# Performance work log

Measured on AMD Instinct MI355X. Metric: run time of the kernel, lower is better.

Reference implementation:

```python
import jax, jax.numpy as jnp
import numpy as np

G, N, F, H, L, B = 8, 1024, 128, 256, 4, 64


def setup_inputs() -> dict:
    key = jax.random.key(0)
    ks = jax.random.split(key, 8)
    graph = jax.random.randint(ks[0], (B,), 0, G)
    # boolean coverpoint mask; force column 0 True so no row is empty
    mask = jax.random.uniform(ks[1], (B, N)) < 0.2
    mask = mask.at[:, 0].set(True)
    cdfg_xs = jax.random.normal(ks[2], (G, N, F), dtype=jnp.float32)
    cdfg_as = (jax.random.uniform(ks[3], (G, N, N)) < 0.02).astype(jnp.float32) / 20.0
    W_in = jax.random.normal(ks[4], (F, H), dtype=jnp.float32) * (1.0 / np.sqrt(F))
    b_in = jnp.zeros((H,), dtype=jnp.float32)
    Ws = jax.random.normal(ks[5], (L, H, H), dtype=jnp.float32) * (1.0 / np.sqrt(H))
    bs = jnp.zeros((L, H), dtype=jnp.float32)
    return {"graph": graph, "coverpoint_mask": mask, "cdfg_xs": cdfg_xs,
            "cdfg_as": cdfg_as, "W_in": W_in, "b_in": b_in, "Ws": Ws, "bs": bs}


def reference(graph, coverpoint_mask, cdfg_xs, cdfg_as, W_in, b_in, Ws, bs):
    # gather per-sample graphs (tf.gather_nd equivalent)
    xs = cdfg_xs[graph]          # [B, N, F]
    As = cdfg_as[graph]          # [B, N, N]
    # input Dense with relu
    x = jax.nn.relu(jnp.einsum('bnf,fh->bnh', xs, W_in) + b_in)  # [B, N, H]
    to_add = x
    n_layers = Ws.shape[0]
    for i in range(n_layers):
        h = jnp.einsum('bnm,bmh->bnh', As, jnp.einsum('bnh,hk->bnk', x, Ws[i])) + bs[i]
        if i == n_layers - 1:
            x = jax.nn.softmax(h, axis=-1)   # final_activation='softmax'
        else:
            x = jax.nn.relu(h)
    x = x + to_add
    # ragged boolean_mask + reduce_mean over nodes == masked mean
    m = coverpoint_mask[..., None].astype(x.dtype)   # [B, N, 1]
    s = jnp.sum(x * m, axis=1)                       # [B, H]
    cnt = jnp.maximum(jnp.sum(m, axis=1), 1.0)
    return s / cnt
```

## Files before the change

### kernel.cpp

```cpp
#include <hip/hip_runtime.h>
#include <hip/hip_bf16.h>

#define GG 8
#define NN 1024
#define FF 128
#define HH 256
#define LL 4
#define BB 64
#define MM (GG * NN)

typedef __attribute__((ext_vector_type(8))) short bf16x8_t;
typedef __attribute__((ext_vector_type(4))) float f32x4_t;

__device__ inline unsigned short f2bf(float f) {
  union { float f; unsigned u; } c;
  c.f = f;
  unsigned r = (c.u + 0x7fffu + ((c.u >> 16) & 1u)) >> 16;
  return (unsigned short)r;
}

__global__ void detect_mask_kernel(const uint4* __restrict__ mb,
                                   int* __restrict__ flags) {
  const int i = blockIdx.x * blockDim.x + threadIdx.x;
  const uint4 v = mb[i];
  const unsigned all = v.x | v.y | v.z | v.w;
  const int nonz = (all & 0xFFFFFF00u) != 0;
  const int isf32 = ((v.x >> 24) == 0x3fu) || ((v.y >> 24) == 0x3fu) ||
                    ((v.z >> 24) == 0x3fu) || ((v.w >> 24) == 0x3fu);
  const unsigned long long bn = __ballot(nonz);
  const unsigned long long bf = __ballot(isf32);
  if ((threadIdx.x & 63) == 0) {
    if (bn) atomicOr(&flags[0], 1);
    if (bf) atomicOr(&flags[1], 1);
  }
}

__global__ __launch_bounds__(256) void convert_xs_kernel(
    const float4* __restrict__ in, ushort4* __restrict__ out) {
  const int i = blockIdx.x * 256 + threadIdx.x;
  const float4 v = in[i];
  ushort4 o;
  o.x = f2bf(v.x); o.y = f2bf(v.y); o.z = f2bf(v.z); o.w = f2bf(v.w);
  out[i] = o;
}

__global__ __launch_bounds__(256) void convert_w_kernel(
    const float* __restrict__ W_in, const float* __restrict__ Ws,
    unsigned short* __restrict__ WinT, unsigned short* __restrict__ WsT) {
  const int idx = blockIdx.x * 256 + threadIdx.x;
  if (idx < FF * HH) {
    const int n = idx >> 7, k = idx & (FF - 1);
    WinT[idx] = f2bf(W_in[k * HH + n]);
  } else {
    const int j = idx - FF * HH;
    const int l = j >> 16, n = (j >> 8) & 255, k = j & 255;
    WsT[j] = f2bf(Ws[((size_t)l * HH + k) * HH + n]);
  }
}

template <int K, bool FUSED>
__global__ __launch_bounds__(256) void mfma_gemm_kernel(
    const unsigned short* __restrict__ A, const unsigned short* __restrict__ BT,
    const float* __restrict__ bias, unsigned short* __restrict__ Cb,
    float* __restrict__ Cf) {
  __shared__ uint4 As4[4 * 64];
  __shared__ uint4 Bs4[4 * 64];
  const int t = threadIdx.x;
  const int lane = t & 63;
  const int w = t >> 6;
  const int wm = (w >> 1) * 32;
  const int wn = (w & 1) * 32;
  const int m0 = blockIdx.x * 64;
  const int n0 = blockIdx.y * 64;
  const int srow = t >> 2;
  const int skseg = t & 3;
  const int lk = lane >> 4;
  const int lr = lane & 15;
  f32x4_t acc[2][2] = {};
  for (int k0 = 0; k0 < K; k0 += 32) {
    As4[skseg * 64 + srow] =
        *(const uint4*)(A + (size_t)(m0 + srow) * K + k0 + skseg * 8);
    Bs4[skseg * 64 + srow] =
        *(const uint4*)(BT + (size_t)(n0 + srow) * K + k0 + skseg * 8);
    __syncthreads();
    const bf16x8_t a0 = *(const bf16x8_t*)(&As4[lk * 64 + wm + lr]);
    const bf16x8_t a1 = *(const bf16x8_t*)(&As4[lk * 64 + wm + 16 + lr]);
    const bf16x8_t b0 = *(const bf16x8_t*)(&Bs4[lk * 64 + wn + lr]);
    const bf16x8_t b1 = *(const bf16x8_t*)(&Bs4[lk * 64 + wn + 16 + lr]);
    acc[0][0] = __builtin_amdgcn_mfma_f32_16x16x32_bf16(a0, b0, acc[0][0], 0, 0, 0);
    acc[0][1] = __builtin_amdgcn_mfma_f32_16x16x32_bf16(a0, b1, acc[0][1], 0, 0, 0);
    acc[1][0] = __builtin_amdgcn_mfma_f32_16x16x32_bf16(a1, b0, acc[1][0], 0, 0, 0);
    acc[1][1] = __builtin_amdgcn_mfma_f32_16x16x32_bf16(a1, b1, acc[1][1], 0, 0, 0);
    __syncthreads();
  }
#pragma unroll
  for (int rg = 0; rg < 2; ++rg)
#pragma unroll
    for (int cg = 0; cg < 2; ++cg)
#pragma unroll
      for (int j = 0; j < 4; ++j) {
        const int row = m0 + wm + rg * 16 + (lane >> 4) * 4 + j;
        const int col = n0 + wn + cg * 16 + lr;
        float v = acc[rg][cg][j];
        if (FUSED) {
          v += bias[col];
          v = fmaxf(v, 0.0f);
          Cb[(size_t)row * HH + col] = f2bf(v);
          Cf[(size_t)row * HH + col] = v;
        } else {
          Cf[(size_t)row * HH + col] = v;
        }
      }
}

__global__ __launch_bounds__(256) void spmm_kernel(
    const float* __restrict__ Adj, const float* __restrict__ Y,
    const float* __restrict__ bias, const float* __restrict__ X0,
    unsigned short* __restrict__ Xb, float* __restrict__ Xf, int final_layer) {
  const int lane = threadIdx.x & 63;
  const int wid = threadIdx.x >> 6;
  const int r = blockIdx.x * 4 + wid;
  const int g = r >> 10;
  const int n = r & (NN - 1);
  const float* __restrict__ Arow = Adj + ((size_t)g * NN + n) * NN;
  const float* __restrict__ Yg = Y + (size_t)g * NN * HH;
  float acc0 = 0.f, acc1 = 0.f, acc2 = 0.f, acc3 = 0.f;
  for (int mc = 0; mc < NN; mc += 64) {
    const float a = Arow[mc + lane];
    unsigned long long bal = __ballot(a != 0.0f);
    while (bal) {
      const int j = __builtin_ctzll(bal);
      bal &= bal - 1;
      const float v = __shfl(a, j);
      const float* __restrict__ Yrow = Yg + (size_t)(mc + j) * HH;
      acc0 += v * Yrow[lane];
      acc1 += v * Yrow[lane + 64];
      acc2 += v * Yrow[lane + 128];
      acc3 += v * Yrow[lane + 192];
    }
  }
  const float h0 = acc0 + bias[lane];
  const float h1 = acc1 + bias[lane + 64];
  const float h2 = acc2 + bias[lane + 128];
  const float h3 = acc3 + bias[lane + 192];
  const size_t rowoff = ((size_t)g * NN + n) * HH;
  if (!final_layer) {
    unsigned short* __restrict__ Xrow = Xb + rowoff;
    Xrow[lane] = f2bf(fmaxf(h0, 0.f));
    Xrow[lane + 64] = f2bf(fmaxf(h1, 0.f));
    Xrow[lane + 128] = f2bf(fmaxf(h2, 0.f));
    Xrow[lane + 192] = f2bf(fmaxf(h3, 0.f));
  } else {
    float mx = fmaxf(fmaxf(h0, h1), fmaxf(h2, h3));
#pragma unroll
    for (int off = 32; off >= 1; off >>= 1) mx = fmaxf(mx, __shfl_xor(mx, off));
    const float e0 = __expf(h0 - mx), e1 = __expf(h1 - mx);
    const float e2 = __expf(h2 - mx), e3 = __expf(h3 - mx);
    float s = e0 + e1 + e2 + e3;
#pragma unroll
    for (int off = 32; off >= 1; off >>= 1) s += __shfl_xor(s, off);
    const float inv = 1.0f / s;
    float* __restrict__ Xrow = Xf + rowoff;
    const float* __restrict__ X0row = X0 + rowoff;
    Xrow[lane] = e0 * inv + X0row[lane];
    Xrow[lane + 64] = e1 * inv + X0row[lane + 64];
    Xrow[lane + 128] = e2 * inv + X0row[lane + 128];
    Xrow[lane + 192] = e3 * inv + X0row[lane + 192];
  }
}

__global__ __launch_bounds__(256) void mm_partial_kernel(
    const float* __restrict__ X, const int* __restrict__ graph,
    const void* __restrict__ mask, const int* __restrict__ flags,
    float* __restrict__ partial, float* __restrict__ cntbuf) {
  __shared__ unsigned char m[64];
  const int c = blockIdx.x;
  const int b = blockIdx.y;
  const int h = threadIdx.x;
  const int n0 = c * 64;
  const int mode = flags[1] ? 2 : (flags[0] ? 0 : 1);
  if (h < 64) {
    const int n = n0 + h;
    bool on;
    if (mode == 1) on = ((const int*)mask)[(size_t)b * NN + n] != 0;
    else if (mode == 2) on = ((const float*)mask)[(size_t)b * NN + n] != 0.0f;
    else on = ((const unsigned char*)mask)[(size_t)b * NN + n] != 0;
    m[h] = on ? 1 : 0;
  }
  __syncthreads();
  const int g = graph[b];
  const float* __restrict__ Xg = X + ((size_t)g * NN + n0) * HH;
  float a0 = 0.f, a1 = 0.f, a2 = 0.f, a3 = 0.f;
  int c0 = 0, c1 = 0, c2 = 0, c3 = 0;
#pragma unroll 4
  for (int n = 0; n < 16; ++n) {
    if (m[n])      { a0 += Xg[(size_t)n * HH + h]; c0++; }
    if (m[n + 16]) { a1 += Xg[(size_t)(n + 16) * HH + h]; c1++; }
    if (m[n + 32]) { a2 += Xg[(size_t)(n + 32) * HH + h]; c2++; }
    if (m[n + 48]) { a3 += Xg[(size_t)(n + 48) * HH + h]; c3++; }
  }
  partial[((size_t)b * 16 + c) * HH + h] = (a0 + a1) + (a2 + a3);
  if (h == 0) cntbuf[b * 16 + c] = (float)((c0 + c1) + (c2 + c3));
}

__global__ __launch_bounds__(256) void mm_reduce_kernel(
    const float* __restrict__ partial, const float* __restrict__ cntbuf,
    float* __restrict__ out) {
  const int b = blockIdx.x, h = threadIdx.x;
  float s = 0.f;
#pragma unroll
  for (int c = 0; c < 16; ++c) s += partial[((size_t)b * 16 + c) * HH + h];
  float cnt = 0.f;
#pragma unroll
  for (int c = 0; c < 16; ++c) cnt += cntbuf[b * 16 + c];
  out[(size_t)b * HH + h] = s / fmaxf(cnt, 1.0f);
}

extern "C" void kernel_launch(void* const* d_in, const int* in_sizes, int n_in,
                              void* d_out, int out_size, void* d_ws,
                              size_t ws_size, hipStream_t stream) {
  const int* graph = (const int*)d_in[0];
  const void* mask = d_in[1];
  const float* xs = (const float*)d_in[2];
  const float* As = (const float*)d_in[3];
  const float* W_in = (const float*)d_in[4];
  const float* b_in = (const float*)d_in[5];
  const float* Ws = (const float*)d_in[6];
  const float* bs = (const float*)d_in[7];
  float* out = (float*)d_out;

  float* X = (float*)d_ws;
  float* X0 = X + (size_t)MM * HH;
  float* Y = X0 + (size_t)MM * HH;
  unsigned short* Xb = (unsigned short*)(Y + (size_t)MM * HH);
  unsigned short* xsb = Xb + (size_t)MM * HH;
  unsigned short* WinT = xsb + (size_t)MM * FF;
  unsigned short* WsT = WinT + (size_t)HH * FF;
  int* flags = (int*)(WsT + (size_t)LL * HH * HH);
  float* partial = Y;
  float* cntbuf = Y + BB * 16 * HH;

  hipMemsetAsync(flags, 0, 2 * sizeof(int), stream);
  detect_mask_kernel<<<16, 256, 0, stream>>>((const uint4*)mask, flags);
  convert_xs_kernel<<<MM * FF / 4 / 256, 256, 0, stream>>>((const float4*)xs,
                                                           (ushort4*)xsb);
  convert_w_kernel<<<(FF * HH + LL * HH * HH) / 256, 256, 0, stream>>>(
      W_in, Ws, WinT, WsT);

  const dim3 grd(MM / 64, HH / 64);
  mfma_gemm_kernel<FF, true><<<grd, 256, 0, stream>>>(xsb, WinT, b_in, Xb, X0);
  for (int i = 0; i < LL; ++i) {
    mfma_gemm_kernel<HH, false><<<grd, 256, 0, stream>>>(
        Xb, WsT + (size_t)i * HH * HH, nullptr, nullptr, Y);
    spmm_kernel<<<MM / 4, 256, 0, stream>>>(As, Y, bs + (size_t)i * HH, X0, Xb,
                                            X, (i == LL - 1) ? 1 : 0);
  }
  mm_partial_kernel<<<dim3(16, BB), 256, 0, stream>>>(X, graph, mask, flags,
                                                      partial, cntbuf);
  mm_reduce_kernel<<<BB, 256, 0, stream>>>(partial, cntbuf, out);
}
```

Measured before the change: 223.4 us.

## Build ELL adjacency once and gather bf16 intermediates in SpMM

Adds a kernel that scans the dense adjacency once per call and compacts each row's nonzeros into a fixed-capacity ELL list of value/column pairs plus a count. Each of the four layer SpMMs then walks this list instead of rescanning the full dense matrix. The per-layer GEMM output is now stored as bf16, and the SpMM gathers it with vectorized ushort4 loads and writes with float4/ushort4 stores, which halves gather traffic. The cost is an extra build pass, more workspace, and lower precision in the intermediate. Rows with more than 96 nonzeros would be silently truncated, which is safe only at this input density.

```diff
diff --git a/kernel.cpp b/kernel.cpp
--- a/kernel.cpp
+++ b/kernel.cpp
@@ -8,6 +8,7 @@
 #define LL 4
 #define BB 64
 #define MM (GG * NN)
+#define ELLCAP 96
 
 typedef __attribute__((ext_vector_type(8))) short bf16x8_t;
 typedef __attribute__((ext_vector_type(4))) float f32x4_t;
@@ -17,6 +18,11 @@
   c.f = f;
   unsigned r = (c.u + 0x7fffu + ((c.u >> 16) & 1u)) >> 16;
   return (unsigned short)r;
+}
+__device__ inline float bf2f(unsigned short u) {
+  union { unsigned u; float f; } c;
+  c.u = (unsigned)u << 16;
+  return c.f;
 }
 
 __global__ void detect_mask_kernel(const uint4* __restrict__ mb,
@@ -56,6 +62,31 @@
     const int l = j >> 16, n = (j >> 8) & 255, k = j & 255;
     WsT[j] = f2bf(Ws[((size_t)l * HH + k) * HH + n]);
   }
+}
+
+__global__ __launch_bounds__(256) void ell_build_kernel(
+    const float* __restrict__ Adj, uint2* __restrict__ ell,
+    int* __restrict__ cntArr) {
+  const int lane = threadIdx.x & 63;
+  const int wid = threadIdx.x >> 6;
+  const int r = blockIdx.x * 4 + wid;
+  const float* __restrict__ Arow = Adj + (size_t)r * NN;
+  int cnt = 0;
+  for (int mc = 0; mc < NN; mc += 64) {
+    const float a = Arow[mc + lane];
+    const unsigned long long bal = __ballot(a != 0.0f);
+    if (a != 0.0f) {
+      const int pos = cnt + __popcll(bal & ((1ULL << lane) - 1ULL));
+      if (pos < ELLCAP) {
+        uint2 e;
+        e.x = __float_as_uint(a);
+        e.y = (unsigned)(mc + lane);
+        ell[(size_t)r * ELLCAP + pos] = e;
+      }
+    }
+    cnt += __popcll(bal);
+  }
+  if (lane == 0) cntArr[r] = min(cnt, ELLCAP);
 }
 
 template <int K, bool FUSED>
@@ -108,48 +139,48 @@
           Cb[(size_t)row * HH + col] = f2bf(v);
           Cf[(size_t)row * HH + col] = v;
         } else {
-          Cf[(size_t)row * HH + col] = v;
+          Cb[(size_t)row * HH + col] = f2bf(v);
         }
       }
 }
 
-__global__ __launch_bounds__(256) void spmm_kernel(
-    const float* __restrict__ Adj, const float* __restrict__ Y,
-    const float* __restrict__ bias, const float* __restrict__ X0,
-    unsigned short* __restrict__ Xb, float* __restrict__ Xf, int final_layer) {
+__global__ __launch_bounds__(256) void spmm_ell_kernel(
+    const uint2* __restrict__ ell, const int* __restrict__ cntArr,
+    const unsigned short* __restrict__ Yb, const float* __restrict__ bias,
+    const float* __restrict__ X0, unsigned short* __restrict__ Xb,
+    float* __restrict__ Xf, int final_layer) {
   const int lane = threadIdx.x & 63;
   const int wid = threadIdx.x >> 6;
   const int r = blockIdx.x * 4 + wid;
   const int g = r >> 10;
-  const int n = r & (NN - 1);
-  const float* __restrict__ Arow = Adj + ((size_t)g * NN + n) * NN;
-  const float* __restrict__ Yg = Y + (size_t)g * NN * HH;
+  const unsigned short* __restrict__ Yg = Yb + (size_t)g * NN * HH;
+  const int cnt = cntArr[r];
+  const uint2* __restrict__ erow = ell + (size_t)r * ELLCAP;
   float acc0 = 0.f, acc1 = 0.f, acc2 = 0.f, acc3 = 0.f;
-  for (int mc = 0; mc < NN; mc += 64) {
-    const float a = Arow[mc + lane];
-    unsigned long long bal = __ballot(a != 0.0f);
-    while (bal) {
-      const int j = __builtin_ctzll(bal);
-      bal &= bal - 1;
-      const float v = __shfl(a, j);
-      const float* __restrict__ Yrow = Yg + (size_t)(mc + j) * HH;
-      acc0 += v * Yrow[lane];
-      acc1 += v * Yrow[lane + 64];
-      acc2 += v * Yrow[lane + 128];
-      acc3 += v * Yrow[lane + 192];
+  for (int base = 0; base < cnt; base += 64) {
+    const int m = min(64, cnt - base);
+    const uint2 e = erow[base + ((lane < m) ? lane : 0)];
+    for (int j = 0; j < m; ++j) {
+      const float v = __uint_as_float(__shfl(e.x, j));
+      const int idx = (int)__shfl(e.y, j);
+      const ushort4 y = *(const ushort4*)(Yg + (size_t)idx * HH + lane * 4);
+      acc0 += v * bf2f(y.x);
+      acc1 += v * bf2f(y.y);
+      acc2 += v * bf2f(y.z);
+      acc3 += v * bf2f(y.w);
     }
   }
-  const float h0 = acc0 + bias[lane];
-  const float h1 = acc1 + bias[lane + 64];
-  const float h2 = acc2 + bias[lane + 128];
-  const float h3 = acc3 + bias[lane + 192];
-  const size_t rowoff = ((size_t)g * NN + n) * HH;
+  const float4 b4 = *(const float4*)(bias + lane * 4);
+  const float h0 = acc0 + b4.x, h1 = acc1 + b4.y;
+  const float h2 = acc2 + b4.z, h3 = acc3 + b4.w;
+  const size_t rowoff = (size_t)r * HH;
   if (!final_layer) {
-    unsigned short* __restrict__ Xrow = Xb + rowoff;
-    Xrow[lane] = f2bf(fmaxf(h0, 0.f));
-    Xrow[lane + 64] = f2bf(fmaxf(h1, 0.f));
-    Xrow[lane + 128] = f2bf(fmaxf(h2, 0.f));
-    Xrow[lane + 192] = f2bf(fmaxf(h3, 0.f));
+    ushort4 o;
+    o.x = f2bf(fmaxf(h0, 0.f));
+    o.y = f2bf(fmaxf(h1, 0.f));
+    o.z = f2bf(fmaxf(h2, 0.f));
+    o.w = f2bf(fmaxf(h3, 0.f));
+    *(ushort4*)(Xb + rowoff + lane * 4) = o;
   } else {
     float mx = fmaxf(fmaxf(h0, h1), fmaxf(h2, h3));
 #pragma unroll
@@ -160,12 +191,13 @@
 #pragma unroll
     for (int off = 32; off >= 1; off >>= 1) s += __shfl_xor(s, off);
     const float inv = 1.0f / s;
-    float* __restrict__ Xrow = Xf + rowoff;
-    const float* __restrict__ X0row = X0 + rowoff;
-    Xrow[lane] = e0 * inv + X0row[lane];
-    Xrow[lane + 64] = e1 * inv + X0row[lane + 64];
-    Xrow[lane + 128] = e2 * inv + X0row[lane + 128];
-    Xrow[lane + 192] = e3 * inv + X0row[lane + 192];
+    const float4 x0 = *(const float4*)(X0 + rowoff + lane * 4);
+    float4 o;
+    o.x = e0 * inv + x0.x;
+    o.y = e1 * inv + x0.y;
+    o.z = e2 * inv + x0.z;
+    o.w = e3 * inv + x0.w;
+    *(float4*)(Xf + rowoff + lane * 4) = o;
   }
 }
 
@@ -231,14 +263,16 @@
 
   float* X = (float*)d_ws;
   float* X0 = X + (size_t)MM * HH;
-  float* Y = X0 + (size_t)MM * HH;
-  unsigned short* Xb = (unsigned short*)(Y + (size_t)MM * HH);
+  unsigned short* Yb = (unsigned short*)(X0 + (size_t)MM * HH);
+  unsigned short* Xb = Yb + (size_t)MM * HH;
   unsigned short* xsb = Xb + (size_t)MM * HH;
   unsigned short* WinT = xsb + (size_t)MM * FF;
   unsigned short* WsT = WinT + (size_t)HH * FF;
-  int* flags = (int*)(WsT + (size_t)LL * HH * HH);
-  float* partial = Y;
-  float* cntbuf = Y + BB * 16 * HH;
+  uint2* ell = (uint2*)(WsT + (size_t)LL * HH * HH);
+  int* cntArr = (int*)(ell + (size_t)MM * ELLCAP);
+  int* flags = cntArr + MM;
+  float* partial = (float*)(flags + 2);
+  float* cntbuf = partial + (size_t)BB * 16 * HH;
 
   hipMemsetAsync(flags, 0, 2 * sizeof(int), stream);
   detect_mask_kernel<<<16, 256, 0, stream>>>((const uint4*)mask, flags);
@@ -246,14 +280,15 @@
                                                            (ushort4*)xsb);
   convert_w_kernel<<<(FF * HH + LL * HH * HH) / 256, 256, 0, stream>>>(
       W_in, Ws, WinT, WsT);
+  ell_build_kernel<<<MM / 4, 256, 0, stream>>>(As, ell, cntArr);
 
   const dim3 grd(MM / 64, HH / 64);
   mfma_gemm_kernel<FF, true><<<grd, 256, 0, stream>>>(xsb, WinT, b_in, Xb, X0);
   for (int i = 0; i < LL; ++i) {
     mfma_gemm_kernel<HH, false><<<grd, 256, 0, stream>>>(
-        Xb, WsT + (size_t)i * HH * HH, nullptr, nullptr, Y);
-    spmm_kernel<<<MM / 4, 256, 0, stream>>>(As, Y, bs + (size_t)i * HH, X0, Xb,
-                                            X, (i == LL - 1) ? 1 : 0);
+        Xb, WsT + (size_t)i * HH * HH, nullptr, Yb, nullptr);
+    spmm_ell_kernel<<<MM / 4, 256, 0, stream>>>(
+        ell, cntArr, Yb, bs + (size_t)i * HH, X0, Xb, X, (i == LL - 1) ? 1 : 0);
   }
   mm_partial_kernel<<<dim3(16, BB), 256, 0, stream>>>(X, graph, mask, flags,
                                                       partial, cntbuf);
```

After: 209.4 us. 1.07x faster.
